# Kernel tuning notes

Measured on AMD Instinct MI355X. Metric: run time of the kernel, lower is better.

The kernel has to match this reference:

```python
import jax, jax.numpy as jnp
import numpy as np

TINY = 1e-8
B, T, D = 128, 32, 400


def _offsets(T):
    offs, off = [], 0
    for lvl in range(T):
        offs.append(off)
        off += T - lvl
    return offs


def _inside_indices(T):
    # For level l, span start i (L = T - l spans), split k in [0, l):
    #   left child  = cell(offs[k] + i)             (span (i, level k))
    #   right child = cell(offs[l-k-1] + i + k + 1) (span (i+k+1, level l-k-1))
    offs = _offsets(T)
    out = {}
    for level in range(1, T):
        L = T - level
        lidx = np.empty((L, level), np.int32)
        ridx = np.empty((L, level), np.int32)
        for i in range(L):
            for k in range(level):
                lidx[i, k] = offs[k] + i
                ridx[i, k] = offs[level - k - 1] + i + k + 1
        out[level] = (jnp.asarray(lidx.reshape(-1)), jnp.asarray(ridx.reshape(-1)))
    return offs, out


def unit_norm(x):
    n = jnp.sqrt(jnp.sum(x * x, axis=-1, keepdims=True))
    return x / jnp.maximum(n, TINY)


def setup_inputs() -> dict:
    key = jax.random.key(0)
    ks = jax.random.split(key, 12)
    sc = 1.0 / np.sqrt(D).astype(np.float32)
    return {
        'x': jax.random.normal(ks[0], (B, T, D), jnp.float32),
        'w_leaf_h': jax.random.normal(ks[1], (D, D), jnp.float32) * sc,
        'b_leaf_h': jax.random.normal(ks[2], (D,), jnp.float32) * sc,
        'w_leaf_c': jax.random.normal(ks[3], (D, D), jnp.float32) * sc,
        'b_leaf_c': jax.random.normal(ks[4], (D,), jnp.float32) * sc,
        'u_lh': jax.random.normal(ks[5], (D, D), jnp.float32) * sc,
        'u_rh': jax.random.normal(ks[6], (D, D), jnp.float32) * sc,
        'b_h': jax.random.normal(ks[7], (D,), jnp.float32) * sc,
        'u_lc': jax.random.normal(ks[8], (D, D), jnp.float32) * sc,
        'u_rc': jax.random.normal(ks[9], (D, D), jnp.float32) * sc,
        'b_c': jax.random.normal(ks[10], (D,), jnp.float32) * sc,
        'w_score': jax.random.normal(ks[11], (D, D), jnp.float32) * sc,
    }


def reference(x, w_leaf_h, b_leaf_h, w_leaf_c, b_leaf_c,
              u_lh, u_rh, b_h, u_lc, u_rc, b_c, w_score):
    Bb, Tt, Dd = x.shape
    offs, idx = _inside_indices(Tt)
    ncells = Tt * (Tt + 1) // 2
    # leaf_transform + unit normalize
    h0 = unit_norm(jnp.tanh(x @ w_leaf_h + b_leaf_h))
    c0 = unit_norm(jnp.tanh(x @ w_leaf_c + b_leaf_c))
    ch = jnp.zeros((Bb, ncells, Dd), x.dtype).at[:, :Tt].set(h0)
    cc = jnp.zeros((Bb, ncells, Dd), x.dtype).at[:, :Tt].set(c0)
    cs = jnp.zeros((Bb, ncells, 1), x.dtype)
    for level in range(1, Tt):  # fixed structural loop over tree levels
        L, N = Tt - level, level
        lidx, ridx = idx[level]
        lh, rh = ch[:, lidx], ch[:, ridx]  # gather: [B, L*N, D]
        lc, rc = cc[:, lidx], cc[:, ridx]
        ls, rs = cs[:, lidx], cs[:, ridx]  # [B, L*N, 1]
        # compose
        h = jnp.tanh(lh @ u_lh + rh @ u_rh + b_h)
        c = jnp.tanh(lc @ u_lc + rc @ u_rc + b_c)
        # bilinear score + child scores, softmax over splits N
        s = jnp.einsum('bnd,de,bne->bn', lh, w_score, rh)[..., None] + ls + rs
        s = s.reshape(Bb, L, N, 1)
        p = jax.nn.softmax(s, axis=2)
        h_agg = unit_norm(jnp.sum(h.reshape(Bb, L, N, Dd) * p, axis=2))
        c_agg = unit_norm(jnp.sum(c.reshape(Bb, L, N, Dd) * p, axis=2))
        s_agg = jnp.sum(s * p, axis=2)
        off = offs[level]
        ch = ch.at[:, off:off + L].set(h_agg)
        cc = cc.at[:, off:off + L].set(c_agg)
        cs = cs.at[:, off:off + L].set(s_agg)
    return ch
```

## Files before the change

kernel.cpp:

```cpp
#include <hip/hip_runtime.h>
#include <hip/hip_bf16.h>
#include <stdint.h>


#define BB 128
#define TT 32
#define DD 400
#define NCELLS 528
#define NW 2000
#define KP 416

typedef __hip_bfloat16 bf16_t;
typedef __attribute__((ext_vector_type(8))) short s8v;
typedef __attribute__((ext_vector_type(4))) float f32x4;

__device__ __forceinline__ int offs_of(int v) { return v * TT - (v * (v - 1)) / 2; }

__device__ __forceinline__ float bf2f(uint16_t u) {
    union { uint32_t i; float f; } v; v.i = ((uint32_t)u) << 16; return v.f;
}
__device__ __forceinline__ uint16_t f2bf(float f) {
    union { float f; uint32_t i; } v; v.f = f;
    uint32_t x = v.i;
    return (uint16_t)((x + 0x7fffu + ((x >> 16) & 1u)) >> 16);
}

__device__ __forceinline__ void block_reduce2(float& a, float& b, float* sred) {
#pragma unroll
    for (int o = 32; o > 0; o >>= 1) { a += __shfl_down(a, o); b += __shfl_down(b, o); }
    int lane = threadIdx.x & 63, w = threadIdx.x >> 6;
    if (lane == 0) { sred[w] = a; sred[4 + w] = b; }
    __syncthreads();
    a = sred[0] + sred[1] + sred[2] + sred[3];
    b = sred[4] + sred[5] + sred[6] + sred[7];
    __syncthreads();
}

__global__ void pack_k(const float* __restrict__ u_lh, const float* __restrict__ u_rh,
                       const float* __restrict__ w_score, const float* __restrict__ u_lc,
                       const float* __restrict__ u_rc, const float* __restrict__ w_leaf_h,
                       const float* __restrict__ w_leaf_c,
                       uint16_t* __restrict__ WT, float* __restrict__ WLEAF) {
    int idx = blockIdx.x * blockDim.x + threadIdx.x;
    const int nWT = NW * KP;
    if (idx < nWT) {
        int n = idx / KP, k = idx - n * KP;
        float v = 0.f;
        if (k < DD) {
            const float* src = (n < 400) ? u_lh : (n < 800) ? u_rh : (n < 1200) ? w_score
                               : (n < 1600) ? u_lc : u_rc;
            int nc = n % 400;
            v = src[k * DD + nc];
        }
        WT[idx] = f2bf(v);
    } else if (idx < nWT + DD * 800) {
        int q = idx - nWT; int d = q / 800, j = q % 800;
        WLEAF[q] = (j < 400) ? w_leaf_h[d * DD + j] : w_leaf_c[d * DD + j - 400];
    }
}

__global__ __launch_bounds__(256)
void gemm_k(const float* __restrict__ A, const float* __restrict__ Bm, int Ncols,
            float* __restrict__ outF) {
    __shared__ float As[8][128];
    __shared__ float Bs[8][128];
    const int t = threadIdx.x;
    const int tile_m = blockIdx.y * 128;
    const int tile_n = blockIdx.x * 128;
    const int lm = t >> 1, lh = t & 1;
    const float* aptr = A + (size_t)(tile_m + lm) * DD + lh * 4;
    const int bk = t >> 5, bn = (t & 31) << 2;
    const int tx = t & 15, ty = t >> 4;
    float acc[8][8];
#pragma unroll
    for (int i = 0; i < 8; i++)
#pragma unroll
        for (int j = 0; j < 8; j++) acc[i][j] = 0.f;

    for (int k0 = 0; k0 < DD; k0 += 8) {
        float4 av = *(const float4*)(aptr + k0);
        float4 bv;
        const int jb = tile_n + bn;
        const float* bp = Bm + (size_t)(k0 + bk) * Ncols + jb;
        if (jb + 3 < Ncols) {
            bv = *(const float4*)bp;
        } else {
            bv.x = (jb + 0 < Ncols) ? bp[0] : 0.f;
            bv.y = (jb + 1 < Ncols) ? bp[1] : 0.f;
            bv.z = (jb + 2 < Ncols) ? bp[2] : 0.f;
            bv.w = (jb + 3 < Ncols) ? bp[3] : 0.f;
        }
        __syncthreads();
        As[lh * 4 + 0][lm] = av.x;
        As[lh * 4 + 1][lm] = av.y;
        As[lh * 4 + 2][lm] = av.z;
        As[lh * 4 + 3][lm] = av.w;
        *(float4*)&Bs[bk][bn] = bv;
        __syncthreads();
#pragma unroll
        for (int k = 0; k < 8; k++) {
            float a[8], b[8];
            *(float4*)&a[0] = *(const float4*)&As[k][ty * 4];
            *(float4*)&a[4] = *(const float4*)&As[k][64 + ty * 4];
            *(float4*)&b[0] = *(const float4*)&Bs[k][tx * 4];
            *(float4*)&b[4] = *(const float4*)&Bs[k][64 + tx * 4];
#pragma unroll
            for (int i = 0; i < 8; i++)
#pragma unroll
                for (int j = 0; j < 8; j++) acc[i][j] = fmaf(a[i], b[j], acc[i][j]);
        }
    }
#pragma unroll
    for (int ih = 0; ih < 2; ih++)
#pragma unroll
        for (int ii = 0; ii < 4; ii++) {
            int r = tile_m + ih * 64 + ty * 4 + ii;
#pragma unroll
            for (int jh = 0; jh < 2; jh++) {
                int colg = tile_n + jh * 64 + tx * 4;
                if (colg >= Ncols) continue;
                float* o = outF + (size_t)r * Ncols + colg;
#pragma unroll
                for (int jj = 0; jj < 4; jj++)
                    if (colg + jj < Ncols) o[jj] = acc[ih * 4 + ii][jh * 4 + jj];
            }
        }
}

__global__ __launch_bounds__(256)
void tgemm_k(const uint16_t* __restrict__ HB, const uint16_t* __restrict__ CB,
             const uint16_t* __restrict__ WT, uint16_t* __restrict__ planes,
             int Lcur, int cellbase) {
    __shared__ short As[128][40];
    __shared__ short Ws[80][40];
    const int t = threadIdx.x, lane = t & 63, w = t >> 6;
    const int n0 = blockIdx.x * 80;
    const int tile_m = blockIdx.y * 128;
    const bool cside = (n0 >= 1200);
    const size_t PL = (size_t)BB * NCELLS * DD;

    const int arow_l = t >> 2, asub = t & 3;
    const uint16_t* aptr[2];
#pragma unroll
    for (int p = 0; p < 2; p++) {
        int gr = tile_m + arow_l + 64 * p;
        int rb = gr / Lcur, ri = gr - rb * Lcur;
        const uint16_t* base = cside ? CB + (size_t)(rb * 32 + ri) * DD
                                     : HB + (size_t)(rb * NCELLS + cellbase + ri) * DD;
        aptr[p] = base + asub * 8;
    }
    const uint16_t* wptr0 = WT + (size_t)(n0 + (t >> 2)) * KP + (t & 3) * 8;
    const uint16_t* wptr1 = WT + (size_t)(n0 + 64 + (t >> 2)) * KP + (t & 3) * 8;

    const int frow = lane & 15, kcol = (lane >> 4) * 8;
    f32x4 acc[2][5];
#pragma unroll
    for (int mi = 0; mi < 2; mi++)
#pragma unroll
        for (int ni = 0; ni < 5; ni++) acc[mi][ni] = (f32x4)(0.f);

    for (int k0 = 0; k0 < KP; k0 += 32) {
        s8v av0 = *(const s8v*)(aptr[0] + k0);
        s8v av1 = *(const s8v*)(aptr[1] + k0);
        s8v wv0 = *(const s8v*)(wptr0 + k0);
        s8v wv1;
        if (t < 64) wv1 = *(const s8v*)(wptr1 + k0);
        __syncthreads();
        *(s8v*)&As[arow_l][asub * 8] = av0;
        *(s8v*)&As[arow_l + 64][asub * 8] = av1;
        *(s8v*)&Ws[t >> 2][(t & 3) * 8] = wv0;
        if (t < 64) *(s8v*)&Ws[64 + (t >> 2)][(t & 3) * 8] = wv1;
        __syncthreads();
        s8v a0 = *(const s8v*)&As[32 * w + frow][kcol];
        s8v a1 = *(const s8v*)&As[32 * w + 16 + frow][kcol];
#pragma unroll
        for (int ni = 0; ni < 5; ni++) {
            s8v bv = *(const s8v*)&Ws[16 * ni + frow][kcol];
            acc[0][ni] = __builtin_amdgcn_mfma_f32_16x16x32_bf16(a0, bv, acc[0][ni], 0, 0, 0);
            acc[1][ni] = __builtin_amdgcn_mfma_f32_16x16x32_bf16(a1, bv, acc[1][ni], 0, 0, 0);
        }
    }

    const int plane = n0 / 400, ncbase = n0 % 400;
    uint16_t* pbase = planes + (size_t)plane * PL;
#pragma unroll
    for (int mi = 0; mi < 2; mi++) {
        int rbase = tile_m + 32 * w + 16 * mi + 4 * (lane >> 4);
#pragma unroll
        for (int i = 0; i < 4; i++) {
            int gr = rbase + i;
            int rb = gr / Lcur, ri = gr - rb * Lcur;
            uint16_t* orow = pbase + (size_t)(rb * NCELLS + cellbase + ri) * DD
                             + ncbase + (lane & 15);
#pragma unroll
            for (int ni = 0; ni < 5; ni++) orow[16 * ni] = f2bf(acc[mi][ni][i]);
        }
    }
}

__global__ __launch_bounds__(256)
void leaf_norm_k(const float* __restrict__ PRE, const float* __restrict__ blh,
                 const float* __restrict__ blc, float* __restrict__ Hchart,
                 uint16_t* __restrict__ HB, uint16_t* __restrict__ CB,
                 float* __restrict__ cs) {
    const int r = blockIdx.x;
    const int b = r >> 5, tt = r & 31;
    const int t = threadIdx.x;
    const int d = t * 2;
    float th0 = 0, th1 = 0, tc0 = 0, tc1 = 0;
    if (d < DD) {
        const float* p = PRE + (size_t)r * 800;
        th0 = tanhf(p[d] + blh[d]);
        th1 = tanhf(p[d + 1] + blh[d + 1]);
        tc0 = tanhf(p[400 + d] + blc[d]);
        tc1 = tanhf(p[400 + d + 1] + blc[d + 1]);
    }
    __shared__ float sred[8];
    float nh = th0 * th0 + th1 * th1, nc = tc0 * tc0 + tc1 * tc1;
    block_reduce2(nh, nc, sred);
    float rh = 1.f / fmaxf(sqrtf(nh), 1e-8f);
    float rc = 1.f / fmaxf(sqrtf(nc), 1e-8f);
    if (d < DD) {
        size_t ho = (size_t)(b * NCELLS + tt) * DD + d;
        float h0 = th0 * rh, h1 = th1 * rh, c0 = tc0 * rc, c1 = tc1 * rc;
        Hchart[ho] = h0; Hchart[ho + 1] = h1;
        *(uint32_t*)(HB + ho) = (uint32_t)f2bf(h0) | ((uint32_t)f2bf(h1) << 16);
        *(uint32_t*)(CB + (size_t)(b * 32 + tt) * DD + d) =
            (uint32_t)f2bf(c0) | ((uint32_t)f2bf(c1) << 16);
    }
    if (t == 0) cs[b * NCELLS + tt] = 0.f;
}

__global__ __launch_bounds__(256)
void level_k(float* __restrict__ Hchart, uint16_t* __restrict__ HB,
             uint16_t* __restrict__ CB, float* __restrict__ cs,
             const uint16_t* __restrict__ planes,
             const float* __restrict__ b_h, const float* __restrict__ b_c, int level) {
    const size_t PL = (size_t)BB * NCELLS * DD;
    const int L = TT - level, N = level;
    const int blk = blockIdx.x;
    const int b = blk / L, i = blk - b * L;
    const int cell = offs_of(level) + i;
    const int t = threadIdx.x, lane = t & 63, w = t >> 6;
    __shared__ float sh_s[32], sh_p[32];
    __shared__ float sred[8];

    const uint16_t* G = planes + 2 * PL;
    for (int k = w; k < N; k += 4) {
        int lcell = offs_of(k) + i;
        int rcell = offs_of(level - k - 1) + i + k + 1;
        const uint16_t* g = G + (size_t)(b * NCELLS + lcell) * DD;
        const uint16_t* hr = HB + (size_t)(b * NCELLS + rcell) * DD;
        float s = 0.f;
        for (int d = lane; d < DD; d += 64) s += bf2f(g[d]) * bf2f(hr[d]);
#pragma unroll
        for (int o = 32; o > 0; o >>= 1) s += __shfl_down(s, o);
        if (lane == 0) sh_s[k] = s + cs[b * NCELLS + lcell] + cs[b * NCELLS + rcell];
    }
    __syncthreads();

    if (t == 0) {
        float m = -1e30f;
        for (int k = 0; k < N; k++) m = fmaxf(m, sh_s[k]);
        float sum = 0.f;
        for (int k = 0; k < N; k++) { float e = expf(sh_s[k] - m); sh_p[k] = e; sum += e; }
        float inv = 1.f / sum, sagg = 0.f;
        for (int k = 0; k < N; k++) { sh_p[k] *= inv; sagg += sh_p[k] * sh_s[k]; }
        cs[b * NCELLS + cell] = sagg;
    }
    __syncthreads();

    float ha0 = 0, ha1 = 0, ca0 = 0, ca1 = 0;
    const int d = t * 2;
    if (d < DD) {
        const float bh0 = b_h[d], bh1 = b_h[d + 1], bc0 = b_c[d], bc1 = b_c[d + 1];
        for (int k = 0; k < N; k++) {
            float p = sh_p[k];
            int lcell = offs_of(k) + i;
            int rcell = offs_of(level - k - 1) + i + k + 1;
            size_t lo = (size_t)(b * NCELLS + lcell) * DD + d;
            size_t ro = (size_t)(b * NCELLS + rcell) * DD + d;
            uint32_t av = *(const uint32_t*)(planes + lo);
            uint32_t bv = *(const uint32_t*)(planes + PL + ro);
            uint32_t ev = *(const uint32_t*)(planes + 3 * PL + lo);
            uint32_t fv = *(const uint32_t*)(planes + 4 * PL + ro);
            ha0 += p * tanhf(bf2f(av & 0xffff) + bf2f(bv & 0xffff) + bh0);
            ha1 += p * tanhf(bf2f(av >> 16) + bf2f(bv >> 16) + bh1);
            ca0 += p * tanhf(bf2f(ev & 0xffff) + bf2f(fv & 0xffff) + bc0);
            ca1 += p * tanhf(bf2f(ev >> 16) + bf2f(fv >> 16) + bc1);
        }
    }
    float nh = ha0 * ha0 + ha1 * ha1, nc = ca0 * ca0 + ca1 * ca1;
    block_reduce2(nh, nc, sred);
    float rh = 1.f / fmaxf(sqrtf(nh), 1e-8f);
    float rc = 1.f / fmaxf(sqrtf(nc), 1e-8f);
    if (d < DD) {
        float h0 = ha0 * rh, h1 = ha1 * rh, c0 = ca0 * rc, c1 = ca1 * rc;
        size_t ho = (size_t)(b * NCELLS + cell) * DD + d;
        Hchart[ho] = h0; Hchart[ho + 1] = h1;
        *(uint32_t*)(HB + ho) = (uint32_t)f2bf(h0) | ((uint32_t)f2bf(h1) << 16);
        *(uint32_t*)(CB + (size_t)(b * 32 + i) * DD + d) =
            (uint32_t)f2bf(c0) | ((uint32_t)f2bf(c1) << 16);
    }
}

extern "C" void kernel_launch(void* const* d_in, const int* in_sizes, int n_in,
                              void* d_out, int out_size, void* d_ws, size_t ws_size,
                              hipStream_t stream) {
    const float* x        = (const float*)d_in[0];
    const float* b_leaf_h = (const float*)d_in[2];
    const float* b_leaf_c = (const float*)d_in[4];
    const float* u_lh     = (const float*)d_in[5];
    const float* u_rh     = (const float*)d_in[6];
    const float* b_h      = (const float*)d_in[7];
    const float* u_lc     = (const float*)d_in[8];
    const float* u_rc     = (const float*)d_in[9];
    const float* b_c      = (const float*)d_in[10];
    const float* w_score  = (const float*)d_in[11];
    const float* w_leaf_h = (const float*)d_in[1];
    const float* w_leaf_c = (const float*)d_in[3];
    float* Hchart = (float*)d_out;

    const size_t PL = (size_t)BB * NCELLS * DD;
    char* p = (char*)d_ws;
    uint16_t* planes = (uint16_t*)p; p += 5 * PL * sizeof(uint16_t);
    uint16_t* HB     = (uint16_t*)p; p += PL * sizeof(uint16_t) + 64;
    uint16_t* CB     = (uint16_t*)p; p += (size_t)BB * 32 * DD * sizeof(uint16_t) + 64;
    float* CS        = (float*)p;    p += (size_t)BB * NCELLS * sizeof(float);
    uint16_t* WT     = (uint16_t*)p; p += (size_t)NW * KP * sizeof(uint16_t);
    float* WLEAF     = (float*)p;    p += (size_t)DD * 800 * sizeof(float);
    float* PRE       = (float*)planes;

    {
        int total = NW * KP + DD * 800;
        pack_k<<<(total + 255) / 256, 256, 0, stream>>>(u_lh, u_rh, w_score, u_lc, u_rc,
                                                        w_leaf_h, w_leaf_c, WT, WLEAF);
    }
    gemm_k<<<dim3(7, 32), 256, 0, stream>>>(x, WLEAF, 800, PRE);
    leaf_norm_k<<<BB * TT, 256, 0, stream>>>(PRE, b_leaf_h, b_leaf_c, Hchart, HB, CB, CS);
    tgemm_k<<<dim3(25, 32), 256, 0, stream>>>(HB, CB, WT, planes, 32, 0);

    int off = TT;
    for (int level = 1; level < TT; ++level) {
        int L = TT - level;
        level_k<<<BB * L, 256, 0, stream>>>(Hchart, HB, CB, CS, planes, b_h, b_c, level);
        if (level < TT - 1) {
            tgemm_k<<<dim3(25, L), 256, 0, stream>>>(HB, CB, WT, planes, L, off);
        }
        off += L;
    }
}
```

Before: 1.733 ms.

## Interleave h/c projection planes and run leaf GEMM on bf16 MFMA path

The left-child h and c projections now share one interleaved buffer, and likewise the right-child ones, so level_k fetches both with a single 8-byte load per side instead of four scattered 4-byte loads. The fp32 SIMT leaf GEMM is replaced by the existing MFMA tgemm kernel in a new mode, with x and the leaf weights packed to bf16 inside pack_k. The score dot-product loop now reads packed bf16 pairs as 32-bit words. In exchange, the leaf projection loses precision because it runs in bf16, and the GEMM epilogue does strided 2-byte stores into the interleaved layout.

```diff
diff --git a/kernel.cpp b/kernel.cpp
--- a/kernel.cpp
+++ b/kernel.cpp
@@ -16,8 +16,8 @@
 
 __device__ __forceinline__ int offs_of(int v) { return v * TT - (v * (v - 1)) / 2; }
 
-__device__ __forceinline__ float bf2f(uint16_t u) {
-    union { uint32_t i; float f; } v; v.i = ((uint32_t)u) << 16; return v.f;
+__device__ __forceinline__ float asf(uint32_t bits) {
+    union { uint32_t i; float f; } v; v.i = bits; return v.f;
 }
 __device__ __forceinline__ uint16_t f2bf(float f) {
     union { float f; uint32_t i; } v; v.f = f;
@@ -39,114 +39,56 @@
 __global__ void pack_k(const float* __restrict__ u_lh, const float* __restrict__ u_rh,
                        const float* __restrict__ w_score, const float* __restrict__ u_lc,
                        const float* __restrict__ u_rc, const float* __restrict__ w_leaf_h,
-                       const float* __restrict__ w_leaf_c,
-                       uint16_t* __restrict__ WT, float* __restrict__ WLEAF) {
+                       const float* __restrict__ w_leaf_c, const float* __restrict__ x,
+                       uint16_t* __restrict__ WT, uint16_t* __restrict__ WLT,
+                       uint16_t* __restrict__ XB) {
     int idx = blockIdx.x * blockDim.x + threadIdx.x;
-    const int nWT = NW * KP;
+    const int nWT = NW * KP, nWLT = 800 * KP, nXB = 4096 * KP;
     if (idx < nWT) {
         int n = idx / KP, k = idx - n * KP;
         float v = 0.f;
         if (k < DD) {
             const float* src = (n < 400) ? u_lh : (n < 800) ? u_rh : (n < 1200) ? w_score
                                : (n < 1600) ? u_lc : u_rc;
-            int nc = n % 400;
-            v = src[k * DD + nc];
+            v = src[k * DD + (n % 400)];
         }
         WT[idx] = f2bf(v);
-    } else if (idx < nWT + DD * 800) {
-        int q = idx - nWT; int d = q / 800, j = q % 800;
-        WLEAF[q] = (j < 400) ? w_leaf_h[d * DD + j] : w_leaf_c[d * DD + j - 400];
-    }
-}
-
-__global__ __launch_bounds__(256)
-void gemm_k(const float* __restrict__ A, const float* __restrict__ Bm, int Ncols,
-            float* __restrict__ outF) {
-    __shared__ float As[8][128];
-    __shared__ float Bs[8][128];
-    const int t = threadIdx.x;
-    const int tile_m = blockIdx.y * 128;
-    const int tile_n = blockIdx.x * 128;
-    const int lm = t >> 1, lh = t & 1;
-    const float* aptr = A + (size_t)(tile_m + lm) * DD + lh * 4;
-    const int bk = t >> 5, bn = (t & 31) << 2;
-    const int tx = t & 15, ty = t >> 4;
-    float acc[8][8];
-#pragma unroll
-    for (int i = 0; i < 8; i++)
-#pragma unroll
-        for (int j = 0; j < 8; j++) acc[i][j] = 0.f;
-
-    for (int k0 = 0; k0 < DD; k0 += 8) {
-        float4 av = *(const float4*)(aptr + k0);
-        float4 bv;
-        const int jb = tile_n + bn;
-        const float* bp = Bm + (size_t)(k0 + bk) * Ncols + jb;
-        if (jb + 3 < Ncols) {
-            bv = *(const float4*)bp;
-        } else {
-            bv.x = (jb + 0 < Ncols) ? bp[0] : 0.f;
-            bv.y = (jb + 1 < Ncols) ? bp[1] : 0.f;
-            bv.z = (jb + 2 < Ncols) ? bp[2] : 0.f;
-            bv.w = (jb + 3 < Ncols) ? bp[3] : 0.f;
-        }
-        __syncthreads();
-        As[lh * 4 + 0][lm] = av.x;
-        As[lh * 4 + 1][lm] = av.y;
-        As[lh * 4 + 2][lm] = av.z;
-        As[lh * 4 + 3][lm] = av.w;
-        *(float4*)&Bs[bk][bn] = bv;
-        __syncthreads();
-#pragma unroll
-        for (int k = 0; k < 8; k++) {
-            float a[8], b[8];
-            *(float4*)&a[0] = *(const float4*)&As[k][ty * 4];
-            *(float4*)&a[4] = *(const float4*)&As[k][64 + ty * 4];
-            *(float4*)&b[0] = *(const float4*)&Bs[k][tx * 4];
-            *(float4*)&b[4] = *(const float4*)&Bs[k][64 + tx * 4];
-#pragma unroll
-            for (int i = 0; i < 8; i++)
-#pragma unroll
-                for (int j = 0; j < 8; j++) acc[i][j] = fmaf(a[i], b[j], acc[i][j]);
-        }
-    }
-#pragma unroll
-    for (int ih = 0; ih < 2; ih++)
-#pragma unroll
-        for (int ii = 0; ii < 4; ii++) {
-            int r = tile_m + ih * 64 + ty * 4 + ii;
-#pragma unroll
-            for (int jh = 0; jh < 2; jh++) {
-                int colg = tile_n + jh * 64 + tx * 4;
-                if (colg >= Ncols) continue;
-                float* o = outF + (size_t)r * Ncols + colg;
-#pragma unroll
-                for (int jj = 0; jj < 4; jj++)
-                    if (colg + jj < Ncols) o[jj] = acc[ih * 4 + ii][jh * 4 + jj];
-            }
-        }
+    } else if (idx < nWT + nWLT) {
+        int q = idx - nWT; int n = q / KP, k = q - n * KP;
+        float v = 0.f;
+        if (k < DD) v = (n < 400) ? w_leaf_h[k * DD + n] : w_leaf_c[k * DD + (n - 400)];
+        WLT[q] = f2bf(v);
+    } else if (idx < nWT + nWLT + nXB) {
+        int q = idx - nWT - nWLT; int r = q / KP, k = q - r * KP;
+        XB[q] = f2bf(k < DD ? x[(size_t)r * DD + k] : 0.f);
+    }
 }
 
 __global__ __launch_bounds__(256)
 void tgemm_k(const uint16_t* __restrict__ HB, const uint16_t* __restrict__ CB,
-             const uint16_t* __restrict__ WT, uint16_t* __restrict__ planes,
-             int Lcur, int cellbase) {
+             const uint16_t* __restrict__ WT,
+             uint16_t* __restrict__ LP, uint16_t* __restrict__ RP, uint16_t* __restrict__ G,
+             float* __restrict__ PREout, int mode, int Lcur, int cellbase) {
     __shared__ short As[128][40];
     __shared__ short Ws[80][40];
     const int t = threadIdx.x, lane = t & 63, w = t >> 6;
     const int n0 = blockIdx.x * 80;
     const int tile_m = blockIdx.y * 128;
-    const bool cside = (n0 >= 1200);
-    const size_t PL = (size_t)BB * NCELLS * DD;
+    const bool cside = (mode == 0) && (n0 >= 1200);
 
     const int arow_l = t >> 2, asub = t & 3;
     const uint16_t* aptr[2];
 #pragma unroll
     for (int p = 0; p < 2; p++) {
         int gr = tile_m + arow_l + 64 * p;
-        int rb = gr / Lcur, ri = gr - rb * Lcur;
-        const uint16_t* base = cside ? CB + (size_t)(rb * 32 + ri) * DD
-                                     : HB + (size_t)(rb * NCELLS + cellbase + ri) * DD;
+        const uint16_t* base;
+        if (mode == 1) {
+            base = HB + (size_t)gr * KP;
+        } else {
+            int rb = gr / Lcur, ri = gr - rb * Lcur;
+            base = cside ? CB + (size_t)(rb * 32 + ri) * DD
+                         : HB + (size_t)(rb * NCELLS + cellbase + ri) * DD;
+        }
         aptr[p] = base + asub * 8;
     }
     const uint16_t* wptr0 = WT + (size_t)(n0 + (t >> 2)) * KP + (t & 3) * 8;
@@ -181,19 +123,32 @@
         }
     }
 
-    const int plane = n0 / 400, ncbase = n0 % 400;
-    uint16_t* pbase = planes + (size_t)plane * PL;
+    const int seg = n0 / 400, ncb = n0 % 400;
+    uint16_t* tb = (seg == 2) ? G : (seg == 0 || seg == 3) ? LP : RP;
+    const int slot = (seg >= 3) ? 1 : 0;
 #pragma unroll
     for (int mi = 0; mi < 2; mi++) {
         int rbase = tile_m + 32 * w + 16 * mi + 4 * (lane >> 4);
 #pragma unroll
         for (int i = 0; i < 4; i++) {
             int gr = rbase + i;
-            int rb = gr / Lcur, ri = gr - rb * Lcur;
-            uint16_t* orow = pbase + (size_t)(rb * NCELLS + cellbase + ri) * DD
-                             + ncbase + (lane & 15);
-#pragma unroll
-            for (int ni = 0; ni < 5; ni++) orow[16 * ni] = f2bf(acc[mi][ni][i]);
+            if (mode == 1) {
+                float* o = PREout + (size_t)gr * 800 + n0 + frow;
+#pragma unroll
+                for (int ni = 0; ni < 5; ni++) o[16 * ni] = acc[mi][ni][i];
+            } else {
+                int rb = gr / Lcur, ri = gr - rb * Lcur;
+                size_t row = (size_t)(rb * NCELLS + cellbase + ri);
+                if (seg == 2) {
+                    uint16_t* o = tb + row * 400 + ncb + frow;
+#pragma unroll
+                    for (int ni = 0; ni < 5; ni++) o[16 * ni] = f2bf(acc[mi][ni][i]);
+                } else {
+                    uint16_t* o = tb + row * 800 + 2 * (ncb + frow) + slot;
+#pragma unroll
+                    for (int ni = 0; ni < 5; ni++) o[32 * ni] = f2bf(acc[mi][ni][i]);
+                }
+            }
         }
     }
 }
@@ -234,9 +189,9 @@
 __global__ __launch_bounds__(256)
 void level_k(float* __restrict__ Hchart, uint16_t* __restrict__ HB,
              uint16_t* __restrict__ CB, float* __restrict__ cs,
-             const uint16_t* __restrict__ planes,
+             const uint16_t* __restrict__ LP, const uint16_t* __restrict__ RP,
+             const uint16_t* __restrict__ G,
              const float* __restrict__ b_h, const float* __restrict__ b_c, int level) {
-    const size_t PL = (size_t)BB * NCELLS * DD;
     const int L = TT - level, N = level;
     const int blk = blockIdx.x;
     const int b = blk / L, i = blk - b * L;
@@ -245,14 +200,17 @@
     __shared__ float sh_s[32], sh_p[32];
     __shared__ float sred[8];
 
-    const uint16_t* G = planes + 2 * PL;
     for (int k = w; k < N; k += 4) {
         int lcell = offs_of(k) + i;
         int rcell = offs_of(level - k - 1) + i + k + 1;
-        const uint16_t* g = G + (size_t)(b * NCELLS + lcell) * DD;
-        const uint16_t* hr = HB + (size_t)(b * NCELLS + rcell) * DD;
+        const uint32_t* g = (const uint32_t*)(G + (size_t)(b * NCELLS + lcell) * DD);
+        const uint32_t* hr = (const uint32_t*)(HB + (size_t)(b * NCELLS + rcell) * DD);
         float s = 0.f;
-        for (int d = lane; d < DD; d += 64) s += bf2f(g[d]) * bf2f(hr[d]);
+        for (int d2 = lane; d2 < 200; d2 += 64) {
+            uint32_t gv = g[d2], hv = hr[d2];
+            s += asf(gv << 16) * asf(hv << 16)
+               + asf(gv & 0xffff0000u) * asf(hv & 0xffff0000u);
+        }
 #pragma unroll
         for (int o = 32; o > 0; o >>= 1) s += __shfl_down(s, o);
         if (lane == 0) sh_s[k] = s + cs[b * NCELLS + lcell] + cs[b * NCELLS + rcell];
@@ -274,20 +232,18 @@
     const int d = t * 2;
     if (d < DD) {
         const float bh0 = b_h[d], bh1 = b_h[d + 1], bc0 = b_c[d], bc1 = b_c[d + 1];
+        const uint16_t* lpb = LP + (size_t)(b * NCELLS) * 800 + 2 * d;
+        const uint16_t* rpb = RP + (size_t)(b * NCELLS) * 800 + 2 * d;
         for (int k = 0; k < N; k++) {
             float p = sh_p[k];
             int lcell = offs_of(k) + i;
             int rcell = offs_of(level - k - 1) + i + k + 1;
-            size_t lo = (size_t)(b * NCELLS + lcell) * DD + d;
-            size_t ro = (size_t)(b * NCELLS + rcell) * DD + d;
-            uint32_t av = *(const uint32_t*)(planes + lo);
-            uint32_t bv = *(const uint32_t*)(planes + PL + ro);
-            uint32_t ev = *(const uint32_t*)(planes + 3 * PL + lo);
-            uint32_t fv = *(const uint32_t*)(planes + 4 * PL + ro);
-            ha0 += p * tanhf(bf2f(av & 0xffff) + bf2f(bv & 0xffff) + bh0);
-            ha1 += p * tanhf(bf2f(av >> 16) + bf2f(bv >> 16) + bh1);
-            ca0 += p * tanhf(bf2f(ev & 0xffff) + bf2f(fv & 0xffff) + bc0);
-            ca1 += p * tanhf(bf2f(ev >> 16) + bf2f(fv >> 16) + bc1);
+            uint2 lv = *(const uint2*)(lpb + (size_t)lcell * 800);
+            uint2 rv = *(const uint2*)(rpb + (size_t)rcell * 800);
+            ha0 += p * tanhf(asf(lv.x << 16) + asf(rv.x << 16) + bh0);
+            ca0 += p * tanhf(asf(lv.x & 0xffff0000u) + asf(rv.x & 0xffff0000u) + bc0);
+            ha1 += p * tanhf(asf(lv.y << 16) + asf(rv.y << 16) + bh1);
+            ca1 += p * tanhf(asf(lv.y & 0xffff0000u) + asf(rv.y & 0xffff0000u) + bc1);
         }
     }
     float nh = ha0 * ha0 + ha1 * ha1, nc = ca0 * ca0 + ca1 * ca1;
@@ -308,7 +264,9 @@
                               void* d_out, int out_size, void* d_ws, size_t ws_size,
                               hipStream_t stream) {
     const float* x        = (const float*)d_in[0];
+    const float* w_leaf_h = (const float*)d_in[1];
     const float* b_leaf_h = (const float*)d_in[2];
+    const float* w_leaf_c = (const float*)d_in[3];
     const float* b_leaf_c = (const float*)d_in[4];
     const float* u_lh     = (const float*)d_in[5];
     const float* u_rh     = (const float*)d_in[6];
@@ -317,35 +275,37 @@
     const float* u_rc     = (const float*)d_in[9];
     const float* b_c      = (const float*)d_in[10];
     const float* w_score  = (const float*)d_in[11];
-    const float* w_leaf_h = (const float*)d_in[1];
-    const float* w_leaf_c = (const float*)d_in[3];
     float* Hchart = (float*)d_out;
 
     const size_t PL = (size_t)BB * NCELLS * DD;
     char* p = (char*)d_ws;
-    uint16_t* planes = (uint16_t*)p; p += 5 * PL * sizeof(uint16_t);
-    uint16_t* HB     = (uint16_t*)p; p += PL * sizeof(uint16_t) + 64;
-    uint16_t* CB     = (uint16_t*)p; p += (size_t)BB * 32 * DD * sizeof(uint16_t) + 64;
-    float* CS        = (float*)p;    p += (size_t)BB * NCELLS * sizeof(float);
-    uint16_t* WT     = (uint16_t*)p; p += (size_t)NW * KP * sizeof(uint16_t);
-    float* WLEAF     = (float*)p;    p += (size_t)DD * 800 * sizeof(float);
-    float* PRE       = (float*)planes;
+    uint16_t* LP = (uint16_t*)p; p += 2 * PL * sizeof(uint16_t);
+    uint16_t* RP = (uint16_t*)p; p += 2 * PL * sizeof(uint16_t);
+    uint16_t* G  = (uint16_t*)p; p += PL * sizeof(uint16_t);
+    uint16_t* HB = (uint16_t*)p; p += PL * sizeof(uint16_t) + 64;
+    uint16_t* CB = (uint16_t*)p; p += (size_t)BB * 32 * DD * sizeof(uint16_t) + 64;
+    float* CS    = (float*)p;    p += (size_t)BB * NCELLS * sizeof(float);
+    uint16_t* WT = (uint16_t*)p; p += (size_t)NW * KP * sizeof(uint16_t);
+    float* PRE    = (float*)LP;
+    uint16_t* WLT = RP;
+    uint16_t* XB  = RP + (size_t)800 * KP;
 
     {
-        int total = NW * KP + DD * 800;
+        int total = NW * KP + 800 * KP + 4096 * KP;
         pack_k<<<(total + 255) / 256, 256, 0, stream>>>(u_lh, u_rh, w_score, u_lc, u_rc,
-                                                        w_leaf_h, w_leaf_c, WT, WLEAF);
-    }
-    gemm_k<<<dim3(7, 32), 256, 0, stream>>>(x, WLEAF, 800, PRE);
+                                                        w_leaf_h, w_leaf_c, x, WT, WLT, XB);
+    }
+    tgemm_k<<<dim3(10, 32), 256, 0, stream>>>(XB, nullptr, WLT, nullptr, nullptr, nullptr,
+                                              PRE, 1, 32, 0);
     leaf_norm_k<<<BB * TT, 256, 0, stream>>>(PRE, b_leaf_h, b_leaf_c, Hchart, HB, CB, CS);
-    tgemm_k<<<dim3(25, 32), 256, 0, stream>>>(HB, CB, WT, planes, 32, 0);
+    tgemm_k<<<dim3(25, 32), 256, 0, stream>>>(HB, CB, WT, LP, RP, G, nullptr, 0, 32, 0);
 
     int off = TT;
     for (int level = 1; level < TT; ++level) {
         int L = TT - level;
-        level_k<<<BB * L, 256, 0, stream>>>(Hchart, HB, CB, CS, planes, b_h, b_c, level);
+        level_k<<<BB * L, 256, 0, stream>>>(Hchart, HB, CB, CS, LP, RP, G, b_h, b_c, level);
         if (level < TT - 1) {
-            tgemm_k<<<dim3(25, L), 256, 0, stream>>>(HB, CB, WT, planes, L, off);
+            tgemm_k<<<dim3(25, L), 256, 0, stream>>>(HB, CB, WT, LP, RP, G, nullptr, 0, L, off);
         }
         off += L;
     }
```

Measured after the change: 1.611 ms. -7.1%, faster.
